# Optimization experiments

Measured on AMD Instinct MI355X. Metric: run time of the kernel, lower is better.

The kernel has to match this reference:

```python
import jax, jax.numpy as jnp
import numpy as np

EPS = 1e-8


def setup_inputs() -> dict:
    key = jax.random.key(0)
    k1, k2, k3, k4 = jax.random.split(key, 4)
    B, C, H, W = 16, 256, 32, 32
    E, V = 512, 8192
    x = jax.random.normal(k1, (B, C, H, W), dtype=jnp.float32)
    w_pre = jax.random.normal(k2, (E, C), dtype=jnp.float32) * 0.05
    b_pre = jax.random.normal(k3, (E,), dtype=jnp.float32) * 0.05
    # embedding init mirrors uniform_(-1/vocab, 1/vocab)
    embedding = jax.random.uniform(k4, (V, E), dtype=jnp.float32, minval=-1.0 / V, maxval=1.0 / V)
    return {"x": x, "w_pre": w_pre, "b_pre": b_pre, "embedding": embedding}


def reference(x, w_pre, b_pre, embedding):
    B, C, H, W = x.shape
    V, E = embedding.shape
    # pre_quant_conv: 1x1 Conv2d == per-pixel linear over channels
    z = jnp.einsum('bchw,ec->behw', x, w_pre) + b_pre[None, :, None, None]  # [B,E,H,W]
    # flatten to (b h w, e)
    z_flat = z.transpose(0, 2, 3, 1).reshape(-1, E)  # [BHW, E]
    zn = z_flat / (EPS + jnp.linalg.norm(z_flat, axis=1, keepdims=True))
    en = embedding / (EPS + jnp.linalg.norm(embedding, axis=1, keepdims=True))
    sims = zn @ en.T  # [BHW, V]
    tokens = jnp.argmax(sims, axis=-1)  # [BHW]
    z_q = embedding[tokens].reshape(B, H, W, E).transpose(0, 3, 1, 2)  # [B,E,H,W]
    # straight-through norm-blend from Tokenizer.forward
    normed_z = z / (EPS + jnp.linalg.norm(z, axis=1, keepdims=True))
    norm_zq = EPS + jnp.linalg.norm(z_q, axis=1, keepdims=True)
    normed_zq = z_q / norm_zq
    decoder_input = (normed_z + jax.lax.stop_gradient(normed_zq - normed_z)) * norm_zq
    return z, z_q, decoder_input, tokens.reshape(B, H * W)
```

## Files before the change

kernel.cpp:

```cpp
#include <hip/hip_runtime.h>
#include <math.h>

#define EPSF 1e-8f
#define MARGIN 4e-3f

constexpr int Bn = 16, Cc = 256, HW = 1024, Ee = 512, Vv = 8192;
constexpr int Mm = Bn * HW;

constexpr long O_Z   = 0;
constexpr long O_ZQ  = 8388608;
constexpr long O_DEC = 16777216;
constexpr long O_TOK = 25165824;

typedef __attribute__((ext_vector_type(8))) short s16x8;
typedef __attribute__((ext_vector_type(4))) short s16x4;
typedef __attribute__((ext_vector_type(8))) _Float16 f16x8;
typedef __attribute__((ext_vector_type(4))) float f32x4;

__device__ __forceinline__ unsigned short f2h(float x) {
    _Float16 h = (_Float16)x;
    return __builtin_bit_cast(unsigned short, h);
}
__device__ __forceinline__ float h2f(unsigned short b) {
    return (float)__builtin_bit_cast(_Float16, b);
}


__global__ void k_wT(const float* __restrict__ w, float* __restrict__ wT) {
    int gid = blockIdx.x * 256 + threadIdx.x;
    int c = gid >> 9, e = gid & 511;
    wT[gid] = w[e * Cc + c];
}

__global__ void k_enB(const float* __restrict__ emb, float* __restrict__ en_inv,
                      float* __restrict__ en_norm, unsigned short* __restrict__ Bhi) {
    int v = blockIdx.x * 4 + (threadIdx.x >> 6);
    int lane = threadIdx.x & 63;
    const float* row = emb + (long)v * Ee + lane * 8;
    float4 d0 = *(const float4*)row;
    float4 d1 = *(const float4*)(row + 4);
    float s = 0.f;
    s = fmaf(d0.x, d0.x, s); s = fmaf(d0.y, d0.y, s);
    s = fmaf(d0.z, d0.z, s); s = fmaf(d0.w, d0.w, s);
    s = fmaf(d1.x, d1.x, s); s = fmaf(d1.y, d1.y, s);
    s = fmaf(d1.z, d1.z, s); s = fmaf(d1.w, d1.w, s);
#pragma unroll
    for (int off = 32; off; off >>= 1) s += __shfl_xor(s, off);
    float n = sqrtf(s);
    float inv = 1.0f / (EPSF + n);
    if (lane == 0) { en_norm[v] = EPSF + n; en_inv[v] = inv; }
    s16x8 h;
    h[0] = (short)f2h(d0.x * inv); h[1] = (short)f2h(d0.y * inv);
    h[2] = (short)f2h(d0.z * inv); h[3] = (short)f2h(d0.w * inv);
    h[4] = (short)f2h(d1.x * inv); h[5] = (short)f2h(d1.y * inv);
    h[6] = (short)f2h(d1.z * inv); h[7] = (short)f2h(d1.w * inv);
    *(s16x8*)(Bhi + (long)v * Ee + lane * 8) = h;
}


__global__ __launch_bounds__(256) void k_gemm1(const float* __restrict__ x,
                                               const float* __restrict__ wT,
                                               const float* __restrict__ bias,
                                               float* __restrict__ z,
                                               float* __restrict__ sumsq_part) {
    __shared__ float As[32][64];
    __shared__ float Bs[32][64];
    int m0 = blockIdx.x * 64;
    int b = m0 >> 10, hw0 = m0 & 1023;
    int e0 = blockIdx.y * 64;
    int t = threadIdx.x;
    int mi = t >> 4, ni = t & 15;
    float acc[4][4] = {};
    for (int c0 = 0; c0 < Cc; c0 += 32) {
#pragma unroll
        for (int q = 0; q < 2; ++q) {
            int f = t + 256 * q;
            int kk = f >> 4, m4 = (f & 15) * 4;
            *(float4*)&As[kk][m4] = *(const float4*)(x + ((long)(b * Cc + c0 + kk)) * HW + hw0 + m4);
            *(float4*)&Bs[kk][m4] = *(const float4*)(wT + (long)(c0 + kk) * Ee + e0 + m4);
        }
        __syncthreads();
#pragma unroll
        for (int kk = 0; kk < 32; ++kk) {
            float4 a = *(float4*)&As[kk][mi * 4];
            float4 bv = *(float4*)&Bs[kk][ni * 4];
            float av[4] = {a.x, a.y, a.z, a.w};
            float bb[4] = {bv.x, bv.y, bv.z, bv.w};
#pragma unroll
            for (int r = 0; r < 4; ++r)
#pragma unroll
                for (int c = 0; c < 4; ++c) acc[r][c] = fmaf(av[r], bb[c], acc[r][c]);
        }
        __syncthreads();
    }
    float sq[4] = {0.f, 0.f, 0.f, 0.f};
#pragma unroll
    for (int c = 0; c < 4; ++c) {
        int e = e0 + ni * 4 + c;
        float be = bias[e];
        float4 o = make_float4(acc[0][c] + be, acc[1][c] + be, acc[2][c] + be, acc[3][c] + be);
        *(float4*)(z + ((long)(b * Ee + e)) * HW + hw0 + mi * 4) = o;
        sq[0] = fmaf(o.x, o.x, sq[0]); sq[1] = fmaf(o.y, o.y, sq[1]);
        sq[2] = fmaf(o.z, o.z, sq[2]); sq[3] = fmaf(o.w, o.w, sq[3]);
    }
#pragma unroll
    for (int r = 0; r < 4; ++r)
#pragma unroll
        for (int off = 1; off < 16; off <<= 1) sq[r] += __shfl_xor(sq[r], off);
    if (ni == 0) {
#pragma unroll
        for (int r = 0; r < 4; ++r)
            sumsq_part[(long)(m0 + mi * 4 + r) * 8 + blockIdx.y] = sq[r];
    }
}


__global__ void k_Asplit(const float* __restrict__ z, const float* __restrict__ sumsq_part,
                         unsigned short* __restrict__ Ahi, unsigned short* __restrict__ Alo,
                         float* __restrict__ inv_zn) {
    __shared__ float tile[64][65];
    __shared__ float inv_s[64];
    int p0 = (blockIdx.x >> 3) * 64;
    int e0 = (blockIdx.x & 7) * 64;
    int b = p0 >> 10, hw0 = p0 & 1023;
    int t = threadIdx.x;
    if (t < 64) {
        const float* sp = sumsq_part + (long)(p0 + t) * 8;
        float s = ((sp[0] + sp[1]) + (sp[2] + sp[3])) + ((sp[4] + sp[5]) + (sp[6] + sp[7]));
        float inv = 1.0f / (EPSF + sqrtf(s));
        inv_s[t] = inv;
        if ((blockIdx.x & 7) == 0) inv_zn[p0 + t] = inv;
    }
#pragma unroll
    for (int q = 0; q < 4; ++q) {
        int f = t + 256 * q;
        int e_l = f >> 4, p4 = (f & 15) * 4;
        float4 d = *(const float4*)(z + ((long)(b * Ee + e0 + e_l)) * HW + hw0 + p4);
        tile[e_l][p4 + 0] = d.x; tile[e_l][p4 + 1] = d.y;
        tile[e_l][p4 + 2] = d.z; tile[e_l][p4 + 3] = d.w;
    }
    __syncthreads();
#pragma unroll
    for (int q = 0; q < 4; ++q) {
        int f = t + 256 * q;
        int p_l = f >> 4, e4 = (f & 15) * 4;
        float inv = inv_s[p_l];
        s16x4 h, lo;
#pragma unroll
        for (int j = 0; j < 4; ++j) {
            float xv = tile[e4 + j][p_l] * inv;
            unsigned short hh = f2h(xv);
            h[j]  = (short)hh;
            lo[j] = (short)f2h(xv - h2f(hh));
        }
        long off = (long)(p0 + p_l) * Ee + e0 + e4;
        *(s16x4*)(Ahi + off) = h;
        *(s16x4*)(Alo + off) = lo;
    }
}


__global__ __launch_bounds__(256, 4) void k_sims(const unsigned short* __restrict__ Ahi,
                                                 const unsigned short* __restrict__ Bhi,
                                                 float* __restrict__ part_v,
                                                 int* __restrict__ part_i,
                                                 float2* __restrict__ extras,
                                                 int* __restrict__ cnt) {
    __shared__ short As[8192];
    __shared__ short Bs[8192];
    __shared__ float red_v[2][2][64];
    __shared__ int   red_i[2][2][64];
    __shared__ float red_m[2][64];
    __shared__ int   red_wi[2][64];

    int t = threadIdx.x;
    int wg = blockIdx.x;
    int xcd = wg & 7, r = wg >> 3;
    int bx = xcd * 16 + (r & 15);
    int by = r >> 4;
    long m0 = (long)bx * 128, n0 = (long)by * 128;

    int wid = t >> 6, l = t & 63;
    int wr = wid >> 1, wc = wid & 1;
    int l15 = l & 15, lg = l >> 4;

    auto stage = [&](const unsigned short* gbase, short* region, long row0, int k0) {
#pragma unroll
        for (int j = 0; j < 4; ++j) {
            int i = j * 256 + t;
            int rr = i >> 3, s = i & 7;
            int sp = s ^ (rr & 7);
            const unsigned short* gp = gbase + (row0 + rr) * Ee + k0 + sp * 8;
            short* lp = region + (long)(j * 256 + (t & ~63)) * 8;
            __builtin_amdgcn_global_load_lds(
                (const __attribute__((address_space(1))) unsigned int*)gp,
                (__attribute__((address_space(3))) unsigned int*)lp, 16, 0, 0);
        }
    };

    f32x4 acc[4][4];
#pragma unroll
    for (int i = 0; i < 4; ++i)
#pragma unroll
        for (int j = 0; j < 4; ++j) acc[i][j] = (f32x4){0.f, 0.f, 0.f, 0.f};

    stage(Ahi, As, m0, 0);
    stage(Bhi, Bs, n0, 0);

    for (int kt = 0; kt < 8; ++kt) {
        __syncthreads();
        s16x8 af[4][2], bf[4][2];
#pragma unroll
        for (int mt = 0; mt < 4; ++mt)
#pragma unroll
            for (int kk = 0; kk < 2; ++kk) {
                int row = wr * 64 + mt * 16 + l15;
                int g = kk * 4 + lg;
                af[mt][kk] = *(const s16x8*)&As[row * 64 + ((g ^ (row & 7)) * 8)];
                int nrow = wc * 64 + mt * 16 + l15;
                bf[mt][kk] = *(const s16x8*)&Bs[nrow * 64 + ((g ^ (nrow & 7)) * 8)];
            }
        __syncthreads();
        if (kt < 7) {
            stage(Ahi, As, m0, (kt + 1) * 64);
            stage(Bhi, Bs, n0, (kt + 1) * 64);
        }
#pragma unroll
        for (int kk = 0; kk < 2; ++kk)
#pragma unroll
            for (int mt = 0; mt < 4; ++mt)
#pragma unroll
                for (int nt = 0; nt < 4; ++nt)
                    acc[mt][nt] = __builtin_amdgcn_mfma_f32_16x16x32_f16(
                        __builtin_bit_cast(f16x8, af[mt][kk]),
                        __builtin_bit_cast(f16x8, bf[nt][kk]), acc[mt][nt], 0, 0, 0);
    }

#pragma unroll
    for (int mt = 0; mt < 4; ++mt)
#pragma unroll
        for (int rg = 0; rg < 4; ++rg) {
            float best = -3e38f; int bi = 0x7FFFFFFF;
#pragma unroll
            for (int nt = 0; nt < 4; ++nt) {
                float val = acc[mt][nt][rg];
                int idx = (int)n0 + wc * 64 + nt * 16 + l15;
                if (val > best) { best = val; bi = idx; }
            }
#pragma unroll
            for (int off = 1; off < 16; off <<= 1) {
                float ov = __shfl_xor(best, off);
                int oi = __shfl_xor(bi, off);
                if (ov > best || (ov == best && oi < bi)) { best = ov; bi = oi; }
            }
            if (l15 == 0) {
                int rloc = mt * 16 + lg * 4 + rg;
                red_v[wr][wc][rloc] = best;
                red_i[wr][wc][rloc] = bi;
            }
        }
    __syncthreads();
    if (t < 128) {
        int wr_ = t >> 6, rloc = t & 63;
        float va = red_v[wr_][0][rloc]; int ia = red_i[wr_][0][rloc];
        float vb = red_v[wr_][1][rloc]; int ib = red_i[wr_][1][rloc];
        if (vb > va || (vb == va && ib < ia)) { va = vb; ia = ib; }
        long m = m0 + wr_ * 64 + rloc;
        part_v[m * 64 + by] = va;
        part_i[m * 64 + by] = ia;
        red_m[wr_][rloc] = va;
        red_wi[wr_][rloc] = ia;
    }
    __syncthreads();
#pragma unroll
    for (int mt = 0; mt < 4; ++mt)
#pragma unroll
        for (int rg = 0; rg < 4; ++rg) {
            int rloc = mt * 16 + lg * 4 + rg;
            float bm = red_m[wr][rloc];
            int wi_ = red_wi[wr][rloc];
            long p = m0 + wr * 64 + rloc;
            float thr = bm - MARGIN;
#pragma unroll
            for (int nt = 0; nt < 4; ++nt) {
                float val = acc[mt][nt][rg];
                int idx = (int)n0 + wc * 64 + nt * 16 + l15;
                if (val >= thr && idx != wi_) {
                    int slot = atomicAdd(&cnt[p], 1);
                    if (slot < 64) extras[p * 64 + slot] = make_float2(val, __int_as_float(idx));
                }
            }
        }
}


__global__ __launch_bounds__(256) void k_pick(const float* __restrict__ part_v,
                                              const int* __restrict__ part_i,
                                              const float2* __restrict__ extras,
                                              const int* __restrict__ cnt,
                                              const unsigned short* __restrict__ Ahi,
                                              const unsigned short* __restrict__ Alo,
                                              const float* __restrict__ emb,
                                              const float* __restrict__ en_inv,
                                              int* __restrict__ tok_i,
                                              float* __restrict__ tok_f) {
    int p = blockIdx.x * 4 + (threadIdx.x >> 6);
    int lane = threadIdx.x & 63;
    float wv = part_v[(long)p * 64 + lane];
    int wi = part_i[(long)p * 64 + lane];
    float m1 = wv;
#pragma unroll
    for (int off = 1; off < 64; off <<= 1) {
        float ov = __shfl_xor(m1, off);
        if (ov > m1) m1 = ov;
    }
    float thr = m1 - MARGIN;
    int n = cnt[p]; if (n > 64) n = 64;
    float ev = -3e38f; int ei = 0;
    if (lane < n) {
        float2 e2 = extras[(long)p * 64 + lane];
        ev = e2.x; ei = __float_as_int(e2.y);
    }
    unsigned long long mw = __ballot(wv >= thr);
    unsigned long long me = __ballot(ev >= thr);
    s16x8 ah = *(const s16x8*)(Ahi + (long)p * Ee + lane * 8);
    s16x8 al = *(const s16x8*)(Alo + (long)p * Ee + lane * 8);
    float a[8];
#pragma unroll
    for (int j = 0; j < 8; ++j)
        a[j] = h2f((unsigned short)ah[j]) + h2f((unsigned short)al[j]);

    float best = -3e38f; int bi = 0x7FFFFFFF;
    auto rescore = [&](int v) {
        const float* er = emb + (long)v * Ee + lane * 8;
        float4 b0 = *(const float4*)er;
        float4 b1 = *(const float4*)(er + 4);
        float s = 0.f;
        s = fmaf(a[0], b0.x, s); s = fmaf(a[1], b0.y, s);
        s = fmaf(a[2], b0.z, s); s = fmaf(a[3], b0.w, s);
        s = fmaf(a[4], b1.x, s); s = fmaf(a[5], b1.y, s);
        s = fmaf(a[6], b1.z, s); s = fmaf(a[7], b1.w, s);
#pragma unroll
        for (int off = 1; off < 64; off <<= 1) s += __shfl_xor(s, off);
        s *= en_inv[v];
        if (s > best || (s == best && v < bi)) { best = s; bi = v; }
    };
    while (mw) {
        int b = __ffsll(mw) - 1; mw &= mw - 1;
        rescore(__shfl(wi, b));
    }
    while (me) {
        int b = __ffsll(me) - 1; me &= me - 1;
        rescore(__shfl(ei, b));
    }
    if (lane == 0) { tok_i[p] = bi; tok_f[p] = (float)bi; }
}


__global__ void k_final(const float* __restrict__ z, const float* __restrict__ emb,
                        const int* __restrict__ tok, const float* __restrict__ inv_zn,
                        const float* __restrict__ en_inv, const float* __restrict__ en_norm,
                        float* __restrict__ zq, float* __restrict__ dec) {
    long gid = (long)blockIdx.x * 256 + threadIdx.x;
    int hw = (int)(gid & 1023);
    int b  = (int)(gid >> 19);
    int p  = (b << 10) | hw;
    int e  = (int)((gid >> 10) & 511);
    int tk = tok[p];
    float zqv = emb[(long)tk * Ee + e];
    float nq  = en_norm[tk];
    float nzq = zqv * en_inv[tk];
    float zv  = z[gid];
    float nz  = zv * inv_zn[p];
    zq[gid]  = zqv;
    dec[gid] = (nz + (nzq - nz)) * nq;
}


extern "C" void kernel_launch(void* const* d_in, const int* in_sizes, int n_in,
                              void* d_out, int out_size, void* d_ws, size_t ws_size,
                              hipStream_t stream) {
    const float* x     = (const float*)d_in[0];
    const float* w_pre = (const float*)d_in[1];
    const float* b_pre = (const float*)d_in[2];
    const float* emb   = (const float*)d_in[3];

    float* out  = (float*)d_out;
    float* z    = out + O_Z;
    float* zq   = out + O_ZQ;
    float* dec  = out + O_DEC;
    float* tokf = out + O_TOK;

    unsigned short* Ahi = (unsigned short*)zq;
    unsigned short* Alo = Ahi + (long)Mm * Ee;
    unsigned short* Bhi = (unsigned short*)dec;
    float*  part_v = dec + 2 * 1024 * 1024;
    int*    part_i = (int*)(dec + 3 * 1024 * 1024);
    float2* extras = (float2*)(dec + 4 * 1024 * 1024);
    int*    cnt    = (int*)(dec + 6 * 1024 * 1024);
    float*  sumsq_part = dec + 6 * 1024 * 1024 + 32768;

    float* ws      = (float*)d_ws;
    float* wT      = ws;
    float* en_inv  = wT + 131072;
    float* en_norm = en_inv + 8192;
    float* inv_zn  = en_norm + 8192;
    int*   tok_i   = (int*)(inv_zn + 16384);

    k_wT<<<512, 256, 0, stream>>>(w_pre, wT);
    k_enB<<<2048, 256, 0, stream>>>(emb, en_inv, en_norm, Bhi);
    dim3 g1(Mm / 64, Ee / 64);
    k_gemm1<<<g1, 256, 0, stream>>>(x, wT, b_pre, z, sumsq_part);
    k_Asplit<<<2048, 256, 0, stream>>>(z, sumsq_part, Ahi, Alo, inv_zn);
    hipMemsetAsync((void*)cnt, 0, Mm * sizeof(int), stream);
    k_sims<<<8192, 256, 0, stream>>>(Ahi, Bhi, part_v, part_i, extras, cnt);
    k_pick<<<Mm / 4, 256, 0, stream>>>(part_v, part_i, extras, cnt, Ahi, Alo, emb,
                                       en_inv, tok_i, tokf);
    k_final<<<(int)(8388608 / 256), 256, 0, stream>>>(z, emb, tok_i, inv_zn, en_inv, en_norm, zq, dec);
}
```

Before: 426.2 us.

## Keep codebook tile resident in LDS and stream A rows directly from global

The similarity GEMM now loads a full 128-row by 512-wide codebook slice into shared memory once per block, then iterates over eight 128-row tiles of z. A fragments are read directly from global memory into registers with a one-step prefetch. Each wave covers a full 128-column strip, which removes the cross-wave shared-memory argmax reduction and extra barriers. This trades a large shared-memory footprint, which limits occupancy to one block per CU, and non-LDS-staged A loads for reduced B re-staging and synchronization.

```diff
diff --git a/kernel.cpp b/kernel.cpp
--- a/kernel.cpp
+++ b/kernel.cpp
@@ -160,91 +160,81 @@
 }
 
 
-__global__ __launch_bounds__(256, 4) void k_sims(const unsigned short* __restrict__ Ahi,
+__global__ __launch_bounds__(512, 2) void k_sims(const unsigned short* __restrict__ Ahi,
                                                  const unsigned short* __restrict__ Bhi,
                                                  float* __restrict__ part_v,
                                                  int* __restrict__ part_i,
                                                  float2* __restrict__ extras,
                                                  int* __restrict__ cnt) {
-    __shared__ short As[8192];
-    __shared__ short Bs[8192];
-    __shared__ float red_v[2][2][64];
-    __shared__ int   red_i[2][2][64];
-    __shared__ float red_m[2][64];
-    __shared__ int   red_wi[2][64];
-
-    int t = threadIdx.x;
-    int wg = blockIdx.x;
-    int xcd = wg & 7, r = wg >> 3;
-    int bx = xcd * 16 + (r & 15);
-    int by = r >> 4;
-    long m0 = (long)bx * 128, n0 = (long)by * 128;
-
-    int wid = t >> 6, l = t & 63;
-    int wr = wid >> 1, wc = wid & 1;
-    int l15 = l & 15, lg = l >> 4;
-
-    auto stage = [&](const unsigned short* gbase, short* region, long row0, int k0) {
-#pragma unroll
-        for (int j = 0; j < 4; ++j) {
-            int i = j * 256 + t;
-            int rr = i >> 3, s = i & 7;
-            int sp = s ^ (rr & 7);
-            const unsigned short* gp = gbase + (row0 + rr) * Ee + k0 + sp * 8;
-            short* lp = region + (long)(j * 256 + (t & ~63)) * 8;
-            __builtin_amdgcn_global_load_lds(
-                (const __attribute__((address_space(1))) unsigned int*)gp,
-                (__attribute__((address_space(3))) unsigned int*)lp, 16, 0, 0);
-        }
-    };
-
-    f32x4 acc[4][4];
-#pragma unroll
-    for (int i = 0; i < 4; ++i)
-#pragma unroll
-        for (int j = 0; j < 4; ++j) acc[i][j] = (f32x4){0.f, 0.f, 0.f, 0.f};
-
-    stage(Ahi, As, m0, 0);
-    stage(Bhi, Bs, n0, 0);
-
-    for (int kt = 0; kt < 8; ++kt) {
-        __syncthreads();
-        s16x8 af[4][2], bf[4][2];
-#pragma unroll
-        for (int mt = 0; mt < 4; ++mt)
+    __shared__ short Bs[128 * 512];
+
+    const int t = threadIdx.x;
+    const int wg = blockIdx.x;
+    const int by = wg & 63;
+    const int mg = wg >> 6;
+    const long n0 = (long)by * 128;
+    const int wid = t >> 6, l = t & 63;
+    const int l15 = l & 15, lg = l >> 4;
+
+#pragma unroll
+    for (int j = 0; j < 16; ++j) {
+        int i = j * 512 + t;
+        int rr = i >> 6;
+        int s  = i & 63;
+        int sp = s ^ (rr & 7);
+        const unsigned short* gp = Bhi + (n0 + rr) * Ee + sp * 8;
+        short* lp = Bs + (long)(j * 512 + (t & ~63)) * 8;
+        __builtin_amdgcn_global_load_lds(
+            (const __attribute__((address_space(1))) unsigned int*)gp,
+            (__attribute__((address_space(3))) unsigned int*)lp, 16, 0, 0);
+    }
+    __syncthreads();
+
+    for (int m = 0; m < 8; ++m) {
+        const long m0 = (long)((mg * 8 + m) * 128);
+        const unsigned short* arow = Ahi + (m0 + wid * 16 + l15) * Ee + lg * 8;
+
+        f32x4 acc[8];
+#pragma unroll
+        for (int nt = 0; nt < 8; ++nt) acc[nt] = (f32x4){0.f, 0.f, 0.f, 0.f};
+
+        s16x8 a0 = *(const s16x8*)(arow);
+        s16x8 a1 = *(const s16x8*)(arow + 32);
+#pragma unroll
+        for (int kt = 0; kt < 8; ++kt) {
+            s16x8 a0n, a1n;
+            if (kt < 7) {
+                a0n = *(const s16x8*)(arow + (kt + 1) * 64);
+                a1n = *(const s16x8*)(arow + (kt + 1) * 64 + 32);
+            }
+            s16x8 bf[8][2];
+#pragma unroll
+            for (int nt = 0; nt < 8; ++nt)
+#pragma unroll
+                for (int kk = 0; kk < 2; ++kk) {
+                    int vrow = nt * 16 + l15;
+                    int slot = kt * 8 + kk * 4 + lg;
+                    bf[nt][kk] = *(const s16x8*)&Bs[vrow * 512 + ((slot ^ (vrow & 7)) * 8)];
+                }
 #pragma unroll
             for (int kk = 0; kk < 2; ++kk) {
-                int row = wr * 64 + mt * 16 + l15;
-                int g = kk * 4 + lg;
-                af[mt][kk] = *(const s16x8*)&As[row * 64 + ((g ^ (row & 7)) * 8)];
-                int nrow = wc * 64 + mt * 16 + l15;
-                bf[mt][kk] = *(const s16x8*)&Bs[nrow * 64 + ((g ^ (nrow & 7)) * 8)];
-            }
-        __syncthreads();
-        if (kt < 7) {
-            stage(Ahi, As, m0, (kt + 1) * 64);
-            stage(Bhi, Bs, n0, (kt + 1) * 64);
-        }
-#pragma unroll
-        for (int kk = 0; kk < 2; ++kk)
-#pragma unroll
-            for (int mt = 0; mt < 4; ++mt)
-#pragma unroll
-                for (int nt = 0; nt < 4; ++nt)
-                    acc[mt][nt] = __builtin_amdgcn_mfma_f32_16x16x32_f16(
-                        __builtin_bit_cast(f16x8, af[mt][kk]),
-                        __builtin_bit_cast(f16x8, bf[nt][kk]), acc[mt][nt], 0, 0, 0);
-    }
-
-#pragma unroll
-    for (int mt = 0; mt < 4; ++mt)
+                s16x8 a = kk ? a1 : a0;
+#pragma unroll
+                for (int nt = 0; nt < 8; ++nt)
+                    acc[nt] = __builtin_amdgcn_mfma_f32_16x16x32_f16(
+                        __builtin_bit_cast(f16x8, a),
+                        __builtin_bit_cast(f16x8, bf[nt][kk]), acc[nt], 0, 0, 0);
+            }
+            if (kt < 7) { a0 = a0n; a1 = a1n; }
+        }
+
 #pragma unroll
         for (int rg = 0; rg < 4; ++rg) {
             float best = -3e38f; int bi = 0x7FFFFFFF;
 #pragma unroll
-            for (int nt = 0; nt < 4; ++nt) {
-                float val = acc[mt][nt][rg];
-                int idx = (int)n0 + wc * 64 + nt * 16 + l15;
+            for (int nt = 0; nt < 8; ++nt) {
+                float val = acc[nt][rg];
+                int idx = (int)n0 + nt * 16 + l15;
                 if (val > best) { best = val; bi = idx; }
             }
 #pragma unroll
@@ -253,44 +243,23 @@
                 int oi = __shfl_xor(bi, off);
                 if (ov > best || (ov == best && oi < bi)) { best = ov; bi = oi; }
             }
+            long p = m0 + wid * 16 + lg * 4 + rg;
             if (l15 == 0) {
-                int rloc = mt * 16 + lg * 4 + rg;
-                red_v[wr][wc][rloc] = best;
-                red_i[wr][wc][rloc] = bi;
-            }
-        }
-    __syncthreads();
-    if (t < 128) {
-        int wr_ = t >> 6, rloc = t & 63;
-        float va = red_v[wr_][0][rloc]; int ia = red_i[wr_][0][rloc];
-        float vb = red_v[wr_][1][rloc]; int ib = red_i[wr_][1][rloc];
-        if (vb > va || (vb == va && ib < ia)) { va = vb; ia = ib; }
-        long m = m0 + wr_ * 64 + rloc;
-        part_v[m * 64 + by] = va;
-        part_i[m * 64 + by] = ia;
-        red_m[wr_][rloc] = va;
-        red_wi[wr_][rloc] = ia;
-    }
-    __syncthreads();
-#pragma unroll
-    for (int mt = 0; mt < 4; ++mt)
-#pragma unroll
-        for (int rg = 0; rg < 4; ++rg) {
-            int rloc = mt * 16 + lg * 4 + rg;
-            float bm = red_m[wr][rloc];
-            int wi_ = red_wi[wr][rloc];
-            long p = m0 + wr * 64 + rloc;
-            float thr = bm - MARGIN;
-#pragma unroll
-            for (int nt = 0; nt < 4; ++nt) {
-                float val = acc[mt][nt][rg];
-                int idx = (int)n0 + wc * 64 + nt * 16 + l15;
-                if (val >= thr && idx != wi_) {
+                part_v[p * 64 + by] = best;
+                part_i[p * 64 + by] = bi;
+            }
+            float thr = best - MARGIN;
+#pragma unroll
+            for (int nt = 0; nt < 8; ++nt) {
+                float val = acc[nt][rg];
+                int idx = (int)n0 + nt * 16 + l15;
+                if (val >= thr && idx != bi) {
                     int slot = atomicAdd(&cnt[p], 1);
                     if (slot < 64) extras[p * 64 + slot] = make_float2(val, __int_as_float(idx));
                 }
             }
         }
+    }
 }
 
 
@@ -413,7 +382,7 @@
     k_gemm1<<<g1, 256, 0, stream>>>(x, wT, b_pre, z, sumsq_part);
     k_Asplit<<<2048, 256, 0, stream>>>(z, sumsq_part, Ahi, Alo, inv_zn);
     hipMemsetAsync((void*)cnt, 0, Mm * sizeof(int), stream);
-    k_sims<<<8192, 256, 0, stream>>>(Ahi, Bhi, part_v, part_i, extras, cnt);
+    k_sims<<<1024, 512, 0, stream>>>(Ahi, Bhi, part_v, part_i, extras, cnt);
     k_pick<<<Mm / 4, 256, 0, stream>>>(part_v, part_i, extras, cnt, Ahi, Alo, emb,
                                        en_inv, tok_i, tokf);
     k_final<<<(int)(8388608 / 256), 256, 0, stream>>>(z, emb, tok_i, inv_zn, en_inv, en_norm, zq, dec);
```

Result: slower. 462.8 us (+8.6%).

## Fuse A-split into GEMM1 epilogue, merge prep kernels, and loop sims over four N tiles

Applied to the files above, without the earlier changes.

The fp16 hi/lo split of z moves into the GEMM1 epilogue and is done on the unnormalized z, so the separate transpose kernel disappears. The argmax margin is scaled by the row norm to keep the same threshold. The weight transpose, embedding normalization and counter zeroing are merged into one prep kernel, which also replaces the memset. The sims kernel now has each block loop over four consecutive 128-wide vocab tiles, reusing the block setup and cutting the grid by four. In exchange, the A tile is reloaded for each N tile and occupancy drops because there are fewer workgroups. Bypassing normalization before the fp16 conversion may also change rounding in the candidate filter.

```diff
diff --git a/kernel.cpp b/kernel.cpp
--- a/kernel.cpp
+++ b/kernel.cpp
@@ -26,16 +26,13 @@
 }
 
 
-__global__ void k_wT(const float* __restrict__ w, float* __restrict__ wT) {
-    int gid = blockIdx.x * 256 + threadIdx.x;
-    int c = gid >> 9, e = gid & 511;
-    wT[gid] = w[e * Cc + c];
-}
-
-__global__ void k_enB(const float* __restrict__ emb, float* __restrict__ en_inv,
-                      float* __restrict__ en_norm, unsigned short* __restrict__ Bhi) {
-    int v = blockIdx.x * 4 + (threadIdx.x >> 6);
-    int lane = threadIdx.x & 63;
+__global__ void k_prep(const float* __restrict__ w, float* __restrict__ wT,
+                       const float* __restrict__ emb, float* __restrict__ en_inv,
+                       float* __restrict__ en_norm, unsigned short* __restrict__ Bhi,
+                       int* __restrict__ cnt) {
+    int b = blockIdx.x, t = threadIdx.x;
+    int v = b * 4 + (t >> 6);
+    int lane = t & 63;
     const float* row = emb + (long)v * Ee + lane * 8;
     float4 d0 = *(const float4*)row;
     float4 d1 = *(const float4*)(row + 4);
@@ -55,6 +52,13 @@
     h[4] = (short)f2h(d1.x * inv); h[5] = (short)f2h(d1.y * inv);
     h[6] = (short)f2h(d1.z * inv); h[7] = (short)f2h(d1.w * inv);
     *(s16x8*)(Bhi + (long)v * Ee + lane * 8) = h;
+    if (b < 512) {
+        int gid = b * 256 + t;
+        int c = gid >> 9, e = gid & 511;
+        wT[gid] = w[e * Cc + c];
+    } else if (b < 576) {
+        cnt[(b - 512) * 256 + t] = 0;
+    }
 }
 
 
@@ -62,6 +66,8 @@
                                                const float* __restrict__ wT,
                                                const float* __restrict__ bias,
                                                float* __restrict__ z,
+                                               unsigned short* __restrict__ Ahi,
+                                               unsigned short* __restrict__ Alo,
                                                float* __restrict__ sumsq_part) {
     __shared__ float As[32][64];
     __shared__ float Bs[32][64];
@@ -93,15 +99,36 @@
         }
         __syncthreads();
     }
-    float sq[4] = {0.f, 0.f, 0.f, 0.f};
+    float ov[4][4];
 #pragma unroll
     for (int c = 0; c < 4; ++c) {
         int e = e0 + ni * 4 + c;
         float be = bias[e];
-        float4 o = make_float4(acc[0][c] + be, acc[1][c] + be, acc[2][c] + be, acc[3][c] + be);
+#pragma unroll
+        for (int r = 0; r < 4; ++r) ov[r][c] = acc[r][c] + be;
+        float4 o = make_float4(ov[0][c], ov[1][c], ov[2][c], ov[3][c]);
         *(float4*)(z + ((long)(b * Ee + e)) * HW + hw0 + mi * 4) = o;
-        sq[0] = fmaf(o.x, o.x, sq[0]); sq[1] = fmaf(o.y, o.y, sq[1]);
-        sq[2] = fmaf(o.z, o.z, sq[2]); sq[3] = fmaf(o.w, o.w, sq[3]);
+    }
+    float sq[4] = {0.f, 0.f, 0.f, 0.f};
+#pragma unroll
+    for (int c = 0; c < 4; ++c) {
+        sq[0] = fmaf(ov[0][c], ov[0][c], sq[0]);
+        sq[1] = fmaf(ov[1][c], ov[1][c], sq[1]);
+        sq[2] = fmaf(ov[2][c], ov[2][c], sq[2]);
+        sq[3] = fmaf(ov[3][c], ov[3][c], sq[3]);
+    }
+#pragma unroll
+    for (int r = 0; r < 4; ++r) {
+        s16x4 h, lo;
+#pragma unroll
+        for (int c = 0; c < 4; ++c) {
+            unsigned short hh = f2h(ov[r][c]);
+            h[c]  = (short)hh;
+            lo[c] = (short)f2h(ov[r][c] - h2f(hh));
+        }
+        long off = (long)(m0 + mi * 4 + r) * Ee + e0 + ni * 4;
+        *(s16x4*)(Ahi + off) = h;
+        *(s16x4*)(Alo + off) = lo;
     }
 #pragma unroll
     for (int r = 0; r < 4; ++r)
@@ -115,53 +142,20 @@
 }
 
 
-__global__ void k_Asplit(const float* __restrict__ z, const float* __restrict__ sumsq_part,
-                         unsigned short* __restrict__ Ahi, unsigned short* __restrict__ Alo,
-                         float* __restrict__ inv_zn) {
-    __shared__ float tile[64][65];
-    __shared__ float inv_s[64];
-    int p0 = (blockIdx.x >> 3) * 64;
-    int e0 = (blockIdx.x & 7) * 64;
-    int b = p0 >> 10, hw0 = p0 & 1023;
-    int t = threadIdx.x;
-    if (t < 64) {
-        const float* sp = sumsq_part + (long)(p0 + t) * 8;
-        float s = ((sp[0] + sp[1]) + (sp[2] + sp[3])) + ((sp[4] + sp[5]) + (sp[6] + sp[7]));
-        float inv = 1.0f / (EPSF + sqrtf(s));
-        inv_s[t] = inv;
-        if ((blockIdx.x & 7) == 0) inv_zn[p0 + t] = inv;
-    }
-#pragma unroll
-    for (int q = 0; q < 4; ++q) {
-        int f = t + 256 * q;
-        int e_l = f >> 4, p4 = (f & 15) * 4;
-        float4 d = *(const float4*)(z + ((long)(b * Ee + e0 + e_l)) * HW + hw0 + p4);
-        tile[e_l][p4 + 0] = d.x; tile[e_l][p4 + 1] = d.y;
-        tile[e_l][p4 + 2] = d.z; tile[e_l][p4 + 3] = d.w;
-    }
-    __syncthreads();
-#pragma unroll
-    for (int q = 0; q < 4; ++q) {
-        int f = t + 256 * q;
-        int p_l = f >> 4, e4 = (f & 15) * 4;
-        float inv = inv_s[p_l];
-        s16x4 h, lo;
-#pragma unroll
-        for (int j = 0; j < 4; ++j) {
-            float xv = tile[e4 + j][p_l] * inv;
-            unsigned short hh = f2h(xv);
-            h[j]  = (short)hh;
-            lo[j] = (short)f2h(xv - h2f(hh));
-        }
-        long off = (long)(p0 + p_l) * Ee + e0 + e4;
-        *(s16x4*)(Ahi + off) = h;
-        *(s16x4*)(Alo + off) = lo;
-    }
+__global__ void k_norm(const float* __restrict__ sumsq_part, float* __restrict__ norm,
+                       float* __restrict__ inv_zn) {
+    int p = blockIdx.x * 256 + threadIdx.x;
+    const float* sp = sumsq_part + (long)p * 8;
+    float s = ((sp[0] + sp[1]) + (sp[2] + sp[3])) + ((sp[4] + sp[5]) + (sp[6] + sp[7]));
+    float nv = EPSF + sqrtf(s);
+    norm[p] = nv;
+    inv_zn[p] = 1.0f / nv;
 }
 
 
 __global__ __launch_bounds__(256, 4) void k_sims(const unsigned short* __restrict__ Ahi,
                                                  const unsigned short* __restrict__ Bhi,
+                                                 const float* __restrict__ norm,
                                                  float* __restrict__ part_v,
                                                  int* __restrict__ part_i,
                                                  float2* __restrict__ extras,
@@ -177,8 +171,9 @@
     int wg = blockIdx.x;
     int xcd = wg & 7, r = wg >> 3;
     int bx = xcd * 16 + (r & 15);
-    int by = r >> 4;
-    long m0 = (long)bx * 128, n0 = (long)by * 128;
+    int quad = r >> 4;
+    long m0 = (long)bx * 128;
+    long nq0 = (long)quad * 512;
 
     int wid = t >> 6, l = t & 63;
     int wr = wid >> 1, wc = wid & 1;
@@ -205,9 +200,9 @@
         for (int j = 0; j < 4; ++j) acc[i][j] = (f32x4){0.f, 0.f, 0.f, 0.f};
 
     stage(Ahi, As, m0, 0);
-    stage(Bhi, Bs, n0, 0);
-
-    for (int kt = 0; kt < 8; ++kt) {
+    stage(Bhi, Bs, nq0, 0);
+
+    for (int kt = 0; kt < 32; ++kt) {
         __syncthreads();
         s16x8 af[4][2], bf[4][2];
 #pragma unroll
@@ -221,9 +216,10 @@
                 bf[mt][kk] = *(const s16x8*)&Bs[nrow * 64 + ((g ^ (nrow & 7)) * 8)];
             }
         __syncthreads();
-        if (kt < 7) {
-            stage(Ahi, As, m0, (kt + 1) * 64);
-            stage(Bhi, Bs, n0, (kt + 1) * 64);
+        if (kt < 31) {
+            int nk = kt + 1;
+            stage(Ahi, As, m0, (nk & 7) * 64);
+            stage(Bhi, Bs, nq0 + (long)(nk >> 3) * 128, (nk & 7) * 64);
         }
 #pragma unroll
         for (int kk = 0; kk < 2; ++kk)
@@ -234,63 +230,71 @@
                     acc[mt][nt] = __builtin_amdgcn_mfma_f32_16x16x32_f16(
                         __builtin_bit_cast(f16x8, af[mt][kk]),
                         __builtin_bit_cast(f16x8, bf[nt][kk]), acc[mt][nt], 0, 0, 0);
-    }
-
-#pragma unroll
-    for (int mt = 0; mt < 4; ++mt)
-#pragma unroll
-        for (int rg = 0; rg < 4; ++rg) {
-            float best = -3e38f; int bi = 0x7FFFFFFF;
-#pragma unroll
-            for (int nt = 0; nt < 4; ++nt) {
-                float val = acc[mt][nt][rg];
-                int idx = (int)n0 + wc * 64 + nt * 16 + l15;
-                if (val > best) { best = val; bi = idx; }
+
+        if ((kt & 7) == 7) {
+            int byv = quad * 4 + (kt >> 3);
+            long n0 = (long)byv * 128;
+#pragma unroll
+            for (int mt = 0; mt < 4; ++mt)
+#pragma unroll
+                for (int rg = 0; rg < 4; ++rg) {
+                    float best = -3e38f; int bi = 0x7FFFFFFF;
+#pragma unroll
+                    for (int nt = 0; nt < 4; ++nt) {
+                        float val = acc[mt][nt][rg];
+                        int idx = (int)n0 + wc * 64 + nt * 16 + l15;
+                        if (val > best) { best = val; bi = idx; }
+                    }
+#pragma unroll
+                    for (int off = 1; off < 16; off <<= 1) {
+                        float ov = __shfl_xor(best, off);
+                        int oi = __shfl_xor(bi, off);
+                        if (ov > best || (ov == best && oi < bi)) { best = ov; bi = oi; }
+                    }
+                    if (l15 == 0) {
+                        int rloc = mt * 16 + lg * 4 + rg;
+                        red_v[wr][wc][rloc] = best;
+                        red_i[wr][wc][rloc] = bi;
+                    }
+                }
+            __syncthreads();
+            if (t < 128) {
+                int wr_ = t >> 6, rloc = t & 63;
+                float va = red_v[wr_][0][rloc]; int ia = red_i[wr_][0][rloc];
+                float vb = red_v[wr_][1][rloc]; int ib = red_i[wr_][1][rloc];
+                if (vb > va || (vb == va && ib < ia)) { va = vb; ia = ib; }
+                long m = m0 + wr_ * 64 + rloc;
+                part_v[m * 64 + byv] = va;
+                part_i[m * 64 + byv] = ia;
+                red_m[wr_][rloc] = va;
+                red_wi[wr_][rloc] = ia;
             }
-#pragma unroll
-            for (int off = 1; off < 16; off <<= 1) {
-                float ov = __shfl_xor(best, off);
-                int oi = __shfl_xor(bi, off);
-                if (ov > best || (ov == best && oi < bi)) { best = ov; bi = oi; }
-            }
-            if (l15 == 0) {
-                int rloc = mt * 16 + lg * 4 + rg;
-                red_v[wr][wc][rloc] = best;
-                red_i[wr][wc][rloc] = bi;
-            }
-        }
-    __syncthreads();
-    if (t < 128) {
-        int wr_ = t >> 6, rloc = t & 63;
-        float va = red_v[wr_][0][rloc]; int ia = red_i[wr_][0][rloc];
-        float vb = red_v[wr_][1][rloc]; int ib = red_i[wr_][1][rloc];
-        if (vb > va || (vb == va && ib < ia)) { va = vb; ia = ib; }
-        long m = m0 + wr_ * 64 + rloc;
-        part_v[m * 64 + by] = va;
-        part_i[m * 64 + by] = ia;
-        red_m[wr_][rloc] = va;
-        red_wi[wr_][rloc] = ia;
-    }
-    __syncthreads();
-#pragma unroll
-    for (int mt = 0; mt < 4; ++mt)
-#pragma unroll
-        for (int rg = 0; rg < 4; ++rg) {
-            int rloc = mt * 16 + lg * 4 + rg;
-            float bm = red_m[wr][rloc];
-            int wi_ = red_wi[wr][rloc];
-            long p = m0 + wr * 64 + rloc;
-            float thr = bm - MARGIN;
-#pragma unroll
-            for (int nt = 0; nt < 4; ++nt) {
-                float val = acc[mt][nt][rg];
-                int idx = (int)n0 + wc * 64 + nt * 16 + l15;
-                if (val >= thr && idx != wi_) {
-                    int slot = atomicAdd(&cnt[p], 1);
-                    if (slot < 64) extras[p * 64 + slot] = make_float2(val, __int_as_float(idx));
+            __syncthreads();
+#pragma unroll
+            for (int mt = 0; mt < 4; ++mt)
+#pragma unroll
+                for (int rg = 0; rg < 4; ++rg) {
+                    int rloc = mt * 16 + lg * 4 + rg;
+                    float bm = red_m[wr][rloc];
+                    int wi_ = red_wi[wr][rloc];
+                    long p = m0 + wr * 64 + rloc;
+                    float thr = bm - MARGIN * norm[p];
+#pragma unroll
+                    for (int nt = 0; nt < 4; ++nt) {
+                        float val = acc[mt][nt][rg];
+                        int idx = (int)n0 + wc * 64 + nt * 16 + l15;
+                        if (val >= thr && idx != wi_) {
+                            int slot = atomicAdd(&cnt[p], 1);
+                            if (slot < 64) extras[p * 64 + slot] = make_float2(val, __int_as_float(idx));
+                        }
+                    }
                 }
-            }
-        }
+#pragma unroll
+            for (int i = 0; i < 4; ++i)
+#pragma unroll
+                for (int j = 0; j < 4; ++j) acc[i][j] = (f32x4){0.f, 0.f, 0.f, 0.f};
+        }
+    }
 }
 
 
@@ -302,6 +306,7 @@
                                               const unsigned short* __restrict__ Alo,
                                               const float* __restrict__ emb,
                                               const float* __restrict__ en_inv,
+                                              const float* __restrict__ norm,
                                               int* __restrict__ tok_i,
                                               float* __restrict__ tok_f) {
     int p = blockIdx.x * 4 + (threadIdx.x >> 6);
@@ -314,7 +319,7 @@
         float ov = __shfl_xor(m1, off);
         if (ov > m1) m1 = ov;
     }
-    float thr = m1 - MARGIN;
+    float thr = m1 - MARGIN * norm[p];
     int n = cnt[p]; if (n > 64) n = 64;
     float ev = -3e38f; int ei = 0;
     if (lane < n) {
@@ -406,15 +411,14 @@
     float* en_norm = en_inv + 8192;
     float* inv_zn  = en_norm + 8192;
     int*   tok_i   = (int*)(inv_zn + 16384);
-
-    k_wT<<<512, 256, 0, stream>>>(w_pre, wT);
-    k_enB<<<2048, 256, 0, stream>>>(emb, en_inv, en_norm, Bhi);
+    float* norm    = (float*)(tok_i + 16384);
+
+    k_prep<<<2048, 256, 0, stream>>>(w_pre, wT, emb, en_inv, en_norm, Bhi, cnt);
     dim3 g1(Mm / 64, Ee / 64);
-    k_gemm1<<<g1, 256, 0, stream>>>(x, wT, b_pre, z, sumsq_part);
-    k_Asplit<<<2048, 256, 0, stream>>>(z, sumsq_part, Ahi, Alo, inv_zn);
-    hipMemsetAsync((void*)cnt, 0, Mm * sizeof(int), stream);
-    k_sims<<<8192, 256, 0, stream>>>(Ahi, Bhi, part_v, part_i, extras, cnt);
+    k_gemm1<<<g1, 256, 0, stream>>>(x, wT, b_pre, z, Ahi, Alo, sumsq_part);
+    k_norm<<<Mm / 256, 256, 0, stream>>>(sumsq_part, norm, inv_zn);
+    k_sims<<<2048, 256, 0, stream>>>(Ahi, Bhi, norm, part_v, part_i, extras, cnt);
     k_pick<<<Mm / 4, 256, 0, stream>>>(part_v, part_i, extras, cnt, Ahi, Alo, emb,
-                                       en_inv, tok_i, tokf);
+                                       en_inv, norm, tok_i, tokf);
     k_final<<<(int)(8388608 / 256), 256, 0, stream>>>(z, emb, tok_i, inv_zn, en_inv, en_norm, zq, dec);
 }
```

After: 1.081 ms. +153.6%, slower.
